# Kernel tuning notes

Measured on AMD Instinct MI355X. Metric: run time of the kernel, lower is better.

The kernel has to match this reference:

```python
import jax, jax.numpy as jnp
import numpy as np

KERNEL_SIZE = 3


def extract_local_features(feature_map, point_coords, kernel_size=KERNEL_SIZE):
    # feature_map: (B,C,H,W); point_coords: (B,N,2) normalized (y,x) in [0,1]
    B, C, H, W = feature_map.shape
    half = kernel_size // 2
    x = (point_coords[..., 1] * (W - 1)).astype(jnp.int32)  # (B,N)
    y = (point_coords[..., 0] * (H - 1)).astype(jnp.int32)
    x_min = jnp.clip(x - half, 0, None)
    x_max = jnp.clip(x + half + 1, None, W)
    y_min = jnp.clip(y - half, 0, None)
    y_max = jnpp_clip = jnp.clip(y + half + 1, None, H)
    y_max = jnp.clip(y + half + 1, None, H)
    # gather a fixed (k,k) window with clamped offsets, mask out-of-window entries
    offs = jnp.arange(kernel_size)  # (k,)
    yy = y_min[..., None] + offs  # (B,N,k) candidate rows
    xx = x_min[..., None] + offs  # (B,N,k)
    y_valid = yy < y_max[..., None]
    x_valid = xx < x_max[..., None]
    yy_c = jnp.clip(yy, 0, H - 1)
    xx_c = jnp.clip(xx, 0, W - 1)
    # flat spatial indices (B,N,k,k)
    flat_idx = yy_c[..., :, None] * W + xx_c[..., None, :]
    valid = (y_valid[..., :, None] & x_valid[..., None, :]).astype(feature_map.dtype)
    fm_flat = feature_map.reshape(B, C, H * W)  # (B,C,HW)

    def per_batch(fm, idx, val):
        # fm: (C,HW); idx,val: (N,k,k)
        g = fm[:, idx.reshape(-1)].reshape(fm.shape[0], *idx.shape)  # (C,N,k,k)
        s = jnp.einsum('cnij,nij->cn', g, val)
        cnt = val.sum(axis=(-1, -2))  # (N,)
        return s / cnt[None, :]

    return jax.vmap(per_batch)(fm_flat, flat_idx, valid)  # (B,C,N)


def point_sample(inp, point_coords):
    # bilinear grid_sample, align_corners=False, coords in [0,1] as (x,y) order
    # per the code: grid = 2*coords - 1; grid_sample uses (x,y) convention
    B, C, H, W = inp.shape
    gx = point_coords[..., 0]  # (B,N) in [0,1]
    gy = point_coords[..., 1]
    # align_corners=False mapping: pix = ((g*2-1)+1)/2 * size - 0.5 = g*size - 0.5
    fx = gx * W - 0.5
    fy = gy * H - 0.5
    x0 = jnp.floor(fx).astype(jnp.int32)
    y0 = jnp.floor(fy).astype(jnp.int32)
    wx = fx - x0
    wy = fy - y0

    def gather(yc, xc):
        inb = ((yc >= 0) & (yc < H) & (xc >= 0) & (xc < W)).astype(inp.dtype)  # (B,N)
        ycc = jnp.clip(yc, 0, H - 1)
        xcc = jnp.clip(xc, 0, W - 1)
        flat = ycc * W + xcc  # (B,N)
        fm = inp.reshape(B, C, H * W)
        g = jax.vmap(lambda f, i: f[:, i])(fm, flat)  # (B,C,N)
        return g * inb[:, None, :]

    v00 = gather(y0, x0)
    v01 = gather(y0, x0 + 1)
    v10 = gather(y0 + 1, x0)
    v11 = gather(y0 + 1, x0 + 1)
    wx_ = wx[:, None, :]
    wy_ = wy[:, None, :]
    out = (v00 * (1 - wx_) * (1 - wy_) + v01 * wx_ * (1 - wy_)
           + v10 * (1 - wx_) * wy_ + v11 * wx_ * wy_)  # (B,C,N)
    return out.transpose(0, 2, 1)  # (B,N,C)


def calculate_uncertainty(mask_logits):
    return -jnp.abs(mask_logits).squeeze(1)  # (B,H,W)


def edge_topk_sampling(edge_masks, uncertainty_map, topk):
    # edge_masks: (B,H,W) {0,1}; uncertainty_map: (B,H,W)
    B, H, W = edge_masks.shape
    NEG = jnp.asarray(-1e30, uncertainty_map.dtype)
    masked_u = jnp.where(edge_masks.reshape(B, -1) == 1,
                         uncertainty_map.reshape(B, -1), NEG)
    vals, idx = jax.lax.top_k(masked_u, topk)  # (B,topk)
    yi = (idx // W).astype(jnp.float32)
    xi = (idx % W).astype(jnp.float32)
    coords = jnp.stack([yi / (H - 1), xi / (W - 1)], axis=-1)  # (B,topk,2) (y,x)
    return idx, coords


def setup_inputs() -> dict:
    key = jax.random.key(0)
    k1, k2, k3, k4 = jax.random.split(key, 4)
    B, C, H, W = 8, 256, 256, 256
    N = 4096
    feature_map = jax.random.normal(k1, (B, C, H, W), dtype=jnp.float32)
    pred_mask = jax.random.normal(k2, (B, 1, H, W), dtype=jnp.float32)
    edge_masks = jax.random.randint(k3, (B, H, W), 0, 2).astype(jnp.int32)
    point_coords = jax.random.uniform(k4, (B, N, 2), dtype=jnp.float32)
    return {"feature_map": feature_map, "pred_mask": pred_mask,
            "edge_masks": edge_masks, "point_coords": point_coords,
            "topk": 4096}


def reference(feature_map, pred_mask, edge_masks, point_coords, topk):
    uncertainty_map = calculate_uncertainty(pred_mask)  # (B,H,W)
    idx, important_coords = edge_topk_sampling(edge_masks, uncertainty_map, topk)
    local_feats = extract_local_features(feature_map, important_coords)  # (B,C,topk)
    sampled = point_sample(feature_map, point_coords)  # (B,N,C)
    return local_feats, sampled, important_coords, idx
```

## Files before the change

kernel.cpp:

```cpp
#include <hip/hip_runtime.h>

#define CC 256
#define HH 256
#define WW 256
#define HWV 65536
#define NN 4096
#define SROWS 18
#define SSTRIDE 256

using u64 = unsigned long long;
using u32 = unsigned int;

__device__ __forceinline__ u32 lbound(const u32* __restrict__ a, u32 n, u32 key) {
    u32 lo = 0, hi = n;
    while (lo < hi) { u32 mid = (lo + hi) >> 1; if (a[mid] < key) lo = mid + 1; else hi = mid; }
    return lo;
}

__global__ void build_keys_k(const float* __restrict__ pm, const int* __restrict__ em,
                             u64* __restrict__ keys) {
    int i = blockIdx.x * blockDim.x + threadIdx.x;
    float f = (em[i] == 1) ? -fabsf(pm[i]) : -1e30f;
    u32 u = __float_as_uint(f);
    u32 k = (u & 0x80000000u) ? ~u : (u | 0x80000000u);
    u32 pix = (u32)i & 0xFFFFu;
    keys[i] = ((u64)k << 16) | (u64)(0xFFFFu - pix);
}

template<int DIRECT>
__global__ __launch_bounds__(1024) void topk_sortpc_k(const float* __restrict__ pm,
                                                      const int* __restrict__ em,
                                                      u64* __restrict__ keys,
                                                      const float* __restrict__ pc,
                                                      u32* __restrict__ stash,
                                                      u32* __restrict__ pixSorted,
                                                      u32* __restrict__ pcSorted,
                                                      float* __restrict__ outCoord,
                                                      float* __restrict__ outIdx) {
    __shared__ u64 sel[NN];
    __shared__ u64 bm[1024];
    __shared__ u32 wp[1024];
    __shared__ u32 s_digit, s_rem, s_cnt;
    const int t = threadIdx.x;
    if (blockIdx.x < 8) {
        const int b = blockIdx.x;
        u64* kb = keys + (size_t)b * HWV;
        const float* pmb = pm + (size_t)b * HWV;
        const int*   emb = em + (size_t)b * HWV;
        u32* hist = (u32*)sel;
        u64 prefix = 0ULL;
        u32 remaining = NN;
        #pragma unroll
        for (int q = 0; q < 4; ++q) hist[t + q * 1024] = 0u;
        __syncthreads();
        for (int i = t; i < HWV; i += 1024) {
            float f = (emb[i] == 1) ? -fabsf(pmb[i]) : -1e30f;
            u32 u = __float_as_uint(f);
            u32 k = (u & 0x80000000u) ? ~u : (u | 0x80000000u);
            u64 K = ((u64)k << 16) | (u64)(0xFFFFu - (u32)i);
            kb[i] = K;
            atomicAdd(&hist[(u32)(K >> 36)], 1u);
        }
        __syncthreads();
        for (int r = 0; r < 4; ++r) {
            int shift = 36 - 12 * r;
            if (r > 0) {
                #pragma unroll
                for (int q = 0; q < 4; ++q) hist[t + q * 1024] = 0u;
                __syncthreads();
                for (int i = t; i < HWV; i += 1024) {
                    u64 K = kb[i];
                    if ((K >> (shift + 12)) == prefix)
                        atomicAdd(&hist[(u32)((K >> shift) & 0xFFFULL)], 1u);
                }
                __syncthreads();
            }
            for (int off = 1; off < 4096; off <<= 1) {
                u32 v[4];
                #pragma unroll
                for (int q = 0; q < 4; ++q) {
                    int i = t + q * 1024;
                    v[q] = hist[i];
                    if (i + off < 4096) v[q] += hist[i + off];
                }
                __syncthreads();
                #pragma unroll
                for (int q = 0; q < 4; ++q) hist[t + q * 1024] = v[q];
                __syncthreads();
            }
            #pragma unroll
            for (int q = 0; q < 4; ++q) {
                int d = t + q * 1024;
                u32 ge = hist[d];
                u32 gt = (d < 4095) ? hist[d + 1] : 0u;
                if (ge >= remaining && gt < remaining) { s_digit = (u32)d; s_rem = remaining - gt; }
            }
            __syncthreads();
            prefix = (prefix << 12) | (u64)s_digit;
            remaining = s_rem;
            __syncthreads();
        }
        if (t == 0) s_cnt = 0u;
        __syncthreads();
        for (int i = t; i < HWV; i += 1024) {
            u64 K = kb[i];
            if (K >= prefix) { u32 p = atomicAdd(&s_cnt, 1u); sel[p] = K; }
        }
        __syncthreads();
        for (int k = 2; k <= NN; k <<= 1) {
            for (int j = k >> 1; j > 0; j >>= 1) {
                for (int i = t; i < NN; i += 1024) {
                    int l = i ^ j;
                    if (l > i) {
                        u64 a = sel[i], c = sel[l];
                        bool asc = ((i & k) == 0);
                        if ((a < c) == asc) { sel[i] = c; sel[l] = a; }
                    }
                }
                __syncthreads();
            }
        }
        bm[t] = 0ULL;
        __syncthreads();
        #pragma unroll
        for (int q = 0; q < 4; ++q) {
            int r = t + q * 1024;
            u32 pix = 0xFFFFu - (u32)(sel[r] & 0xFFFFULL);
            if (DIRECT) {
                u32 yi = pix >> 8, xi = pix & 255u;
                outCoord[((size_t)b * NN + r) * 2 + 0] = (float)yi / 255.0f;
                outCoord[((size_t)b * NN + r) * 2 + 1] = (float)xi / 255.0f;
                outIdx[b * NN + r] = (float)pix;
            } else {
                stash[b * NN + r] = pix;
            }
            atomicOr(&bm[pix >> 6], 1ULL << (pix & 63));
        }
        __syncthreads();
        wp[t] = (u32)__popcll(bm[t]);
        __syncthreads();
        for (int off = 1; off < 1024; off <<= 1) {
            u32 v = wp[t];
            if (t >= off) v += wp[t - off];
            __syncthreads();
            wp[t] = v;
            __syncthreads();
        }
        #pragma unroll
        for (int q = 0; q < 4; ++q) {
            int r = t + q * 1024;
            u32 pix = 0xFFFFu - (u32)(sel[r] & 0xFFFFULL);
            int w = (int)(pix >> 6);
            u32 pos = wp[w] - (u32)__popcll(bm[w])
                    + (u32)__popcll(bm[w] & ((1ULL << (pix & 63)) - 1ULL));
            pixSorted[b * NN + pos] = (pix << 12) | (u32)r;
        }
    } else {
        const int b = blockIdx.x - 8;
        u32* cellArr = (u32*)sel;
        u32* hist256 = wp;
        u32* cnt     = (u32*)bm;
        if (t < 256) { hist256[t] = 0u; cnt[t] = 0u; }
        __syncthreads();
        for (int n = t; n < NN; n += 1024) {
            float gx = pc[((size_t)b * NN + n) * 2 + 0];
            float gy = pc[((size_t)b * NN + n) * 2 + 1];
            float fx = gx * 256.0f - 0.5f;
            float fy = gy * 256.0f - 0.5f;
            int x0 = (int)floorf(fx), y0 = (int)floorf(fy);
            int xc = min(max(x0, 0), 255), yc = min(max(y0, 0), 255);
            cellArr[n] = ((u32)(yc * 256 + xc) << 12) | (u32)n;
            atomicAdd(&hist256[yc], 1u);
        }
        __syncthreads();
        for (int off = 1; off < 256; off <<= 1) {
            u32 v = 0;
            if (t < 256) { v = hist256[t]; if (t >= off) v += hist256[t - off]; }
            __syncthreads();
            if (t < 256) hist256[t] = v;
            __syncthreads();
        }
        for (int n = t; n < NN; n += 1024) {
            u32 pk = cellArr[n];
            u32 yc = pk >> 20;
            u32 base = (yc > 0) ? hist256[yc - 1] : 0u;
            u32 pos = base + atomicAdd(&cnt[yc], 1u);
            pcSorted[b * NN + pos] = pk;
        }
    }
}

#define STAGE_DMA(plane, smbuf) \
    { _Pragma("unroll") \
      for (int u = 0; u < 5; ++u) { \
        int idx = t + u * 256; \
        if (idx < SROWS * 64) { \
            int row = idx >> 6; \
            int gr = min(max(rStart + row, 0), HH - 1); \
            const float* gsrc = (plane) + gr * WW + ((idx & 63) << 2); \
            float* ldst = (smbuf) + row * SSTRIDE; \
            __builtin_amdgcn_global_load_lds( \
                (const __attribute__((address_space(1))) void*)gsrc, \
                (__attribute__((address_space(3))) void*)ldst, 16, 0, 0); \
        } } }

__global__ __launch_bounds__(256) void plane_gather_k(const float* __restrict__ fm,
                                                      const float* __restrict__ pc,
                                                      const u32* __restrict__ pixSorted,
                                                      const u32* __restrict__ pcSorted,
                                                      float* __restrict__ outLc,
                                                      float* __restrict__ outSc) {
    __shared__ float smA[SROWS * SSTRIDE];
    __shared__ float smB[SROWS * SSTRIDE];
    const int band = blockIdx.x, c0 = blockIdx.y * 32, b = blockIdx.z;
    const int t = threadIdx.x;
    const int rStart = band * 16 - 1;
    const u32 keyLo = (u32)band << 24, keyHi = (u32)(band + 1) << 24;
    const u32* aL = pixSorted + b * NN;
    const u32* aS = pcSorted + b * NN;
    u32 loL = lbound(aL, NN, keyLo), cL = lbound(aL, NN, keyHi) - loL;
    u32 loS = lbound(aS, NN, keyLo), cS = lbound(aS, NN, keyHi) - loS;
    const float* planes = fm + ((size_t)b * CC + c0) * HWV;
    const float* pcb = pc + (size_t)b * NN * 2;

    int  Lo0 = 0, Lc2 = 0, Lr2 = 0;   float Lwc = 0, Lwr = 0, Lic = 0;
    int  Mo0 = 0, Mc2 = 0, Mr2 = 0;   float Mwc = 0, Mwr = 0, Mic = 0;
    int  So0 = 0, Sr1 = 0;            float Sv0 = 0, Sv1 = 0, Sw0 = 0, Sw1 = 0;
    int  To0 = 0, Tr1 = 0;            float Tv0 = 0, Tv1 = 0, Tw0 = 0, Tw1 = 0;
    {
        u32 jl = (u32)t;
        if (jl < cL) {
            u32 pix = aL[loL + jl] >> 12;
            int yi = (int)(pix >> 8), xi = (int)(pix & 255u);
            float cy = (float)yi / 255.0f, cx = (float)xi / 255.0f;
            int x = (int)(cx * 255.0f), y = (int)(cy * 255.0f);
            int x_min = max(x - 1, 0), wid = min(x + 2, WW) - x_min;
            int y_min = max(y - 1, 0), hgt = min(y + 2, HH) - y_min;
            Lo0 = (y_min - rStart) * SSTRIDE + x_min;
            Lc2 = (wid == 3) ? 2 : 0;  Lwc = (wid == 3) ? 1.0f : 0.0f;
            Lr2 = ((hgt == 3) ? 2 : 0) * SSTRIDE;  Lwr = (hgt == 3) ? 1.0f : 0.0f;
            Lic = 1.0f / (float)(wid * hgt);
        }
        jl = 256u + (u32)t;
        if (jl < cL) {
            u32 pix = aL[loL + jl] >> 12;
            int yi = (int)(pix >> 8), xi = (int)(pix & 255u);
            float cy = (float)yi / 255.0f, cx = (float)xi / 255.0f;
            int x = (int)(cx * 255.0f), y = (int)(cy * 255.0f);
            int x_min = max(x - 1, 0), wid = min(x + 2, WW) - x_min;
            int y_min = max(y - 1, 0), hgt = min(y + 2, HH) - y_min;
            Mo0 = (y_min - rStart) * SSTRIDE + x_min;
            Mc2 = (wid == 3) ? 2 : 0;  Mwc = (wid == 3) ? 1.0f : 0.0f;
            Mr2 = ((hgt == 3) ? 2 : 0) * SSTRIDE;  Mwr = (hgt == 3) ? 1.0f : 0.0f;
            Mic = 1.0f / (float)(wid * hgt);
        }
        u32 js = (u32)t;
        if (js < cS) {
            u32 sn = aS[loS + js] & 0xFFFu;
            float gx = pcb[2 * sn + 0], gy = pcb[2 * sn + 1];
            float fx = gx * 256.0f - 0.5f, fy = gy * 256.0f - 0.5f;
            float fx0 = floorf(fx), fy0 = floorf(fy);
            int x0 = (int)fx0, y0 = (int)fy0;
            float wx = fx - fx0, wy = fy - fy0;
            int xb = min(max(x0, 0), WW - 2);
            if (x0 < 0)            { Sv0 = wx;        Sv1 = 0.0f; }
            else if (x0 >= WW - 1) { Sv0 = 0.0f;      Sv1 = 1.0f - wx; }
            else                   { Sv0 = 1.0f - wx; Sv1 = wx; }
            Sw0 = (y0 >= 0)     ? (1.0f - wy) : 0.0f;
            Sw1 = (y0 + 1 < HH) ? wy          : 0.0f;
            int yc0 = min(max(y0, 0), HH - 1), yc1 = min(max(y0 + 1, 0), HH - 1);
            So0 = (yc0 - rStart) * SSTRIDE + xb;
            Sr1 = (yc1 - yc0) * SSTRIDE;
        }
        js = 256u + (u32)t;
        if (js < cS) {
            u32 sn = aS[loS + js] & 0xFFFu;
            float gx = pcb[2 * sn + 0], gy = pcb[2 * sn + 1];
            float fx = gx * 256.0f - 0.5f, fy = gy * 256.0f - 0.5f;
            float fx0 = floorf(fx), fy0 = floorf(fy);
            int x0 = (int)fx0, y0 = (int)fy0;
            float wx = fx - fx0, wy = fy - fy0;
            int xb = min(max(x0, 0), WW - 2);
            if (x0 < 0)            { Tv0 = wx;        Tv1 = 0.0f; }
            else if (x0 >= WW - 1) { Tv0 = 0.0f;      Tv1 = 1.0f - wx; }
            else                   { Tv0 = 1.0f - wx; Tv1 = wx; }
            Tw0 = (y0 >= 0)     ? (1.0f - wy) : 0.0f;
            Tw1 = (y0 + 1 < HH) ? wy          : 0.0f;
            int yc0 = min(max(y0, 0), HH - 1), yc1 = min(max(y0 + 1, 0), HH - 1);
            To0 = (yc0 - rStart) * SSTRIDE + xb;
            Tr1 = (yc1 - yc0) * SSTRIDE;
        }
    }

    STAGE_DMA(planes, smA)
    __syncthreads();

    #pragma unroll 1
    for (int j = 0; j < 32; ++j) {
        const float* sm = (j & 1) ? smB : smA;
        if (j + 1 < 32) {
            const float* np = planes + (size_t)(j + 1) * HWV;
            float* nb = ((j + 1) & 1) ? smB : smA;
            STAGE_DMA(np, nb)
        }
        float* oL = outLc + ((size_t)(b * CC + c0 + j)) * NN + loL;
        float* oS = outSc + ((size_t)(b * CC + c0 + j)) * NN + loS;
        if ((u32)t < cL) {
            float r0 = sm[Lo0] + sm[Lo0 + 1] + Lwc * sm[Lo0 + Lc2];
            float r1 = sm[Lo0 + SSTRIDE] + sm[Lo0 + SSTRIDE + 1] + Lwc * sm[Lo0 + SSTRIDE + Lc2];
            int o2 = Lo0 + Lr2;
            float r2 = sm[o2] + sm[o2 + 1] + Lwc * sm[o2 + Lc2];
            oL[t] = (r0 + r1 + Lwr * r2) * Lic;
        }
        if (256u + (u32)t < cL) {
            float r0 = sm[Mo0] + sm[Mo0 + 1] + Mwc * sm[Mo0 + Mc2];
            float r1 = sm[Mo0 + SSTRIDE] + sm[Mo0 + SSTRIDE + 1] + Mwc * sm[Mo0 + SSTRIDE + Mc2];
            int o2 = Mo0 + Mr2;
            float r2 = sm[o2] + sm[o2 + 1] + Mwc * sm[o2 + Mc2];
            oL[256 + t] = (r0 + r1 + Mwr * r2) * Mic;
        }
        if ((u32)t < cS) {
            oS[t] = Sw0 * (sm[So0] * Sv0 + sm[So0 + 1] * Sv1)
                  + Sw1 * (sm[So0 + Sr1] * Sv0 + sm[So0 + Sr1 + 1] * Sv1);
        }
        if (256u + (u32)t < cS) {
            oS[256 + t] = Tw0 * (sm[To0] * Tv0 + sm[To0 + 1] * Tv1)
                        + Tw1 * (sm[To0 + Tr1] * Tv0 + sm[To0 + Tr1 + 1] * Tv1);
        }
        __syncthreads();
    }

    for (u32 jl = 512 + (u32)t; jl < cL; jl += 256) {
        u32 pix = aL[loL + jl] >> 12;
        int yi = (int)(pix >> 8), xi = (int)(pix & 255u);
        float cy = (float)yi / 255.0f, cx = (float)xi / 255.0f;
        int x = (int)(cx * 255.0f), y = (int)(cy * 255.0f);
        int x_min = max(x - 1, 0), x_max = min(x + 2, WW);
        int y_min = max(y - 1, 0), y_max = min(y + 2, HH);
        float ic = 1.0f / (float)((x_max - x_min) * (y_max - y_min));
        for (int j = 0; j < 32; ++j) {
            const float* p = planes + (size_t)j * HWV;
            float s = 0.0f;
            for (int yy = y_min; yy < y_max; ++yy)
                for (int xx = x_min; xx < x_max; ++xx) s += p[yy * WW + xx];
            outLc[((size_t)(b * CC + c0 + j)) * NN + loL + jl] = s * ic;
        }
    }
    for (u32 js = 512 + (u32)t; js < cS; js += 256) {
        u32 sn = aS[loS + js] & 0xFFFu;
        float gx = pcb[2 * sn + 0], gy = pcb[2 * sn + 1];
        float fx = gx * 256.0f - 0.5f, fy = gy * 256.0f - 0.5f;
        float fx0 = floorf(fx), fy0 = floorf(fy);
        int x0 = (int)fx0, y0 = (int)fy0;
        float wx = fx - fx0, wy = fy - fy0;
        int xb = min(max(x0, 0), WW - 2);
        float v0, v1, r0, r1;
        if (x0 < 0)            { v0 = wx;        v1 = 0.0f; }
        else if (x0 >= WW - 1) { v0 = 0.0f;      v1 = 1.0f - wx; }
        else                   { v0 = 1.0f - wx; v1 = wx; }
        r0 = (y0 >= 0)     ? (1.0f - wy) : 0.0f;
        r1 = (y0 + 1 < HH) ? wy          : 0.0f;
        int yc0 = min(max(y0, 0), HH - 1), yc1 = min(max(y0 + 1, 0), HH - 1);
        int o0 = yc0 * WW + xb, o1 = yc1 * WW + xb;
        for (int j = 0; j < 32; ++j) {
            const float* p = planes + (size_t)j * HWV;
            outSc[((size_t)(b * CC + c0 + j)) * NN + loS + js] =
                r0 * (p[o0] * v0 + p[o0 + 1] * v1) + r1 * (p[o1] * v0 + p[o1 + 1] * v1);
        }
    }
}

__global__ __launch_bounds__(256) void unpermL_k(const float* __restrict__ outLc,
                                                 const u32* __restrict__ pixSorted,
                                                 float* __restrict__ outL) {
    __shared__ float row[NN];
    const int c = blockIdx.x, b = blockIdx.y;
    const int t = threadIdx.x;
    const float* in = outLc + ((size_t)(b * CC + c)) * NN;
    for (int j = t; j < NN; j += 256)
        row[pixSorted[b * NN + j] & 0xFFFu] = in[j];
    __syncthreads();
    float* o = outL + ((size_t)(b * CC + c)) * NN;
    for (int i = t; i < NN; i += 256) o[i] = row[i];
}

__global__ __launch_bounds__(256) void unpermS_k(const float* __restrict__ outSc,
                                                 const u32* __restrict__ pcSorted,
                                                 float* __restrict__ outS) {
    __shared__ float tile[32][257];
    __shared__ u32 ns[256];
    const int j0 = blockIdx.x * 256, c0 = blockIdx.y * 32, b = blockIdx.z;
    const int t = threadIdx.x;
    ns[t] = pcSorted[b * NN + j0 + t] & 0xFFFu;
    for (int i = 0; i < 32; ++i)
        tile[i][t] = outSc[((size_t)(b * CC + c0 + i)) * NN + j0 + t];
    __syncthreads();
    for (int idx = t; idx < 8192; idx += 256) {
        int p = idx >> 5, k = idx & 31;
        outS[((size_t)b * NN + ns[p]) * CC + c0 + k] = tile[k][p];
    }
}

template<int DIRECT>
__global__ __launch_bounds__(1024) void topk_sortpc_old_k(const u64* __restrict__ keys,
                                                          const float* __restrict__ pc,
                                                          u32* __restrict__ stash,
                                                          u32* __restrict__ pixSorted,
                                                          u32* __restrict__ pcSorted,
                                                          float* __restrict__ outCoord,
                                                          float* __restrict__ outIdx) {
    __shared__ u64 sel[NN];
    __shared__ u64 bm[1024];
    __shared__ u32 wp[1024];
    __shared__ u32 s_digit, s_rem, s_cnt;
    const int t = threadIdx.x;
    if (blockIdx.x < 8) {
        const int b = blockIdx.x;
        const u64* kb = keys + (size_t)b * HWV;
        u32* hist = (u32*)sel;
        u64 prefix = 0ULL;
        u32 remaining = NN;
        for (int r = 0; r < 4; ++r) {
            int shift = 36 - 12 * r;
            #pragma unroll
            for (int q = 0; q < 4; ++q) hist[t + q * 1024] = 0u;
            __syncthreads();
            for (int i = t; i < HWV; i += 1024) {
                u64 K = kb[i];
                if ((K >> (shift + 12)) == prefix)
                    atomicAdd(&hist[(u32)((K >> shift) & 0xFFFULL)], 1u);
            }
            __syncthreads();
            for (int off = 1; off < 4096; off <<= 1) {
                u32 v[4];
                #pragma unroll
                for (int q = 0; q < 4; ++q) {
                    int i = t + q * 1024;
                    v[q] = hist[i];
                    if (i + off < 4096) v[q] += hist[i + off];
                }
                __syncthreads();
                #pragma unroll
                for (int q = 0; q < 4; ++q) hist[t + q * 1024] = v[q];
                __syncthreads();
            }
            #pragma unroll
            for (int q = 0; q < 4; ++q) {
                int d = t + q * 1024;
                u32 ge = hist[d];
                u32 gt = (d < 4095) ? hist[d + 1] : 0u;
                if (ge >= remaining && gt < remaining) { s_digit = (u32)d; s_rem = remaining - gt; }
            }
            __syncthreads();
            prefix = (prefix << 12) | (u64)s_digit;
            remaining = s_rem;
            __syncthreads();
        }
        if (t == 0) s_cnt = 0u;
        __syncthreads();
        for (int i = t; i < HWV; i += 1024) {
            u64 K = kb[i];
            if (K >= prefix) { u32 p = atomicAdd(&s_cnt, 1u); sel[p] = K; }
        }
        __syncthreads();
        for (int k = 2; k <= NN; k <<= 1) {
            for (int j = k >> 1; j > 0; j >>= 1) {
                for (int i = t; i < NN; i += 1024) {
                    int l = i ^ j;
                    if (l > i) {
                        u64 a = sel[i], c = sel[l];
                        bool asc = ((i & k) == 0);
                        if ((a < c) == asc) { sel[i] = c; sel[l] = a; }
                    }
                }
                __syncthreads();
            }
        }
        bm[t] = 0ULL;
        __syncthreads();
        #pragma unroll
        for (int q = 0; q < 4; ++q) {
            int r = t + q * 1024;
            u32 pix = 0xFFFFu - (u32)(sel[r] & 0xFFFFULL);
            if (DIRECT) {
                u32 yi = pix >> 8, xi = pix & 255u;
                outCoord[((size_t)b * NN + r) * 2 + 0] = (float)yi / 255.0f;
                outCoord[((size_t)b * NN + r) * 2 + 1] = (float)xi / 255.0f;
                outIdx[b * NN + r] = (float)pix;
            } else {
                stash[b * NN + r] = pix;
            }
            atomicOr(&bm[pix >> 6], 1ULL << (pix & 63));
        }
        __syncthreads();
        wp[t] = (u32)__popcll(bm[t]);
        __syncthreads();
        for (int off = 1; off < 1024; off <<= 1) {
            u32 v = wp[t];
            if (t >= off) v += wp[t - off];
            __syncthreads();
            wp[t] = v;
            __syncthreads();
        }
        #pragma unroll
        for (int q = 0; q < 4; ++q) {
            int r = t + q * 1024;
            u32 pix = 0xFFFFu - (u32)(sel[r] & 0xFFFFULL);
            int w = (int)(pix >> 6);
            u32 pos = wp[w] - (u32)__popcll(bm[w])
                    + (u32)__popcll(bm[w] & ((1ULL << (pix & 63)) - 1ULL));
            pixSorted[b * NN + pos] = (pix << 12) | (u32)r;
        }
    } else {
        const int b = blockIdx.x - 8;
        u32* cellArr = (u32*)sel;
        u32* hist256 = wp;
        u32* cnt     = (u32*)bm;
        if (t < 256) { hist256[t] = 0u; cnt[t] = 0u; }
        __syncthreads();
        for (int n = t; n < NN; n += 1024) {
            float gx = pc[((size_t)b * NN + n) * 2 + 0];
            float gy = pc[((size_t)b * NN + n) * 2 + 1];
            float fx = gx * 256.0f - 0.5f;
            float fy = gy * 256.0f - 0.5f;
            int x0 = (int)floorf(fx), y0 = (int)floorf(fy);
            int xc = min(max(x0, 0), 255), yc = min(max(y0, 0), 255);
            cellArr[n] = ((u32)(yc * 256 + xc) << 12) | (u32)n;
            atomicAdd(&hist256[yc], 1u);
        }
        __syncthreads();
        for (int off = 1; off < 256; off <<= 1) {
            u32 v = 0;
            if (t < 256) { v = hist256[t]; if (t >= off) v += hist256[t - off]; }
            __syncthreads();
            if (t < 256) hist256[t] = v;
            __syncthreads();
        }
        for (int n = t; n < NN; n += 1024) {
            u32 pk = cellArr[n];
            u32 yc = pk >> 20;
            u32 base = (yc > 0) ? hist256[yc - 1] : 0u;
            u32 pos = base + atomicAdd(&cnt[yc], 1u);
            pcSorted[b * NN + pos] = pk;
        }
    }
}

template<int MODE>
__global__ __launch_bounds__(256, 4) void gather_k(const float* __restrict__ fm,
                                                   const float* __restrict__ pc,
                                                   const u32* __restrict__ pixSorted,
                                                   const u32* __restrict__ pcSorted,
                                                   float* __restrict__ outLp,
                                                   float* __restrict__ outS) {
    __shared__ float tile[256][33];
    __shared__ u32 pidx[256];
    const int b = blockIdx.z, j0 = blockIdx.x * 256, t = threadIdx.x;
    bool doL; int c0;
    if (MODE == 1) { doL = true; c0 = blockIdx.y * 32; }
    else { doL = false; c0 = blockIdx.y * 32; }
    const float* planes = fm + ((size_t)b * CC + c0) * HWV;
    if (doL) {
        u32 packed = pixSorted[b * NN + j0 + t];
        u32 pix = packed >> 12;
        pidx[t] = packed & 0xFFFu;
        int yi = (int)(pix >> 8), xi = (int)(pix & 255u);
        float cy = (float)yi / 255.0f, cx = (float)xi / 255.0f;
        int x = (int)(cx * 255.0f), y = (int)(cy * 255.0f);
        int x_min = max(x - 1, 0), x_max = min(x + 2, WW);
        int y_min = max(y - 1, 0), y_max = min(y + 2, HH);
        int base = min(x_min & ~3, WW - 8);
        float w8[8];
        #pragma unroll
        for (int i = 0; i < 8; ++i)
            w8[i] = (base + i >= x_min && base + i < x_max) ? 1.0f : 0.0f;
        float wr2 = (y_min + 2 < y_max) ? 1.0f : 0.0f;
        int o0 = y_min * WW + base, o1 = o0 + WW;
        int o2 = min(y_min + 2, HH - 1) * WW + base;
        float invc = 1.0f / (float)((x_max - x_min) * (y_max - y_min));
        #pragma unroll 2
        for (int j = 0; j < 32; ++j) {
            const float* p = planes + (size_t)j * HWV;
            float4 a0 = *(const float4*)(p + o0), b0 = *(const float4*)(p + o0 + 4);
            float4 a1 = *(const float4*)(p + o1), b1 = *(const float4*)(p + o1 + 4);
            float4 a2 = *(const float4*)(p + o2), b2 = *(const float4*)(p + o2 + 4);
            float s0 = a0.x * w8[0] + a0.y * w8[1] + a0.z * w8[2] + a0.w * w8[3]
                     + b0.x * w8[4] + b0.y * w8[5] + b0.z * w8[6] + b0.w * w8[7];
            float s1 = a1.x * w8[0] + a1.y * w8[1] + a1.z * w8[2] + a1.w * w8[3]
                     + b1.x * w8[4] + b1.y * w8[5] + b1.z * w8[6] + b1.w * w8[7];
            float s2 = a2.x * w8[0] + a2.y * w8[1] + a2.z * w8[2] + a2.w * w8[3]
                     + b2.x * w8[4] + b2.y * w8[5] + b2.z * w8[6] + b2.w * w8[7];
            tile[t][j] = (s0 + s1 + wr2 * s2) * invc;
        }
        __syncthreads();
        for (int idx = t; idx < 8192; idx += 256) {
            int p = idx >> 5, k = idx & 31;
            outLp[((size_t)b * NN + pidx[p]) * CC + c0 + k] = tile[p][k];
        }
    } else {
        int n = (int)(pcSorted[b * NN + j0 + t] & 0xFFFu);
        pidx[t] = (u32)n;
        float gx = pc[((size_t)b * NN + n) * 2 + 0];
        float gy = pc[((size_t)b * NN + n) * 2 + 1];
        float fx = gx * 256.0f - 0.5f, fy = gy * 256.0f - 0.5f;
        float fx0 = floorf(fx), fy0 = floorf(fy);
        int x0 = (int)fx0, y0 = (int)fy0;
        float wx = fx - fx0, wy = fy - fy0;
        int xb = min(max(x0, 0), WW - 2);
        float wv0, wv1;
        if (x0 < 0)            { wv0 = wx;        wv1 = 0.0f; }
        else if (x0 >= WW - 1) { wv0 = 0.0f;      wv1 = 1.0f - wx; }
        else                   { wv0 = 1.0f - wx; wv1 = wx; }
        float wr0 = (y0 >= 0)     ? (1.0f - wy) : 0.0f;
        float wr1 = (y0 + 1 < HH) ? wy          : 0.0f;
        int yc0 = min(max(y0, 0), HH - 1), yc1 = min(max(y0 + 1, 0), HH - 1);
        int o0 = yc0 * WW + xb, o1 = yc1 * WW + xb;
        #pragma unroll 4
        for (int j = 0; j < 32; ++j) {
            const float* p = planes + (size_t)j * HWV;
            tile[t][j] = wr0 * (p[o0] * wv0 + p[o0 + 1] * wv1)
                       + wr1 * (p[o1] * wv0 + p[o1 + 1] * wv1);
        }
        __syncthreads();
        for (int idx = t; idx < 8192; idx += 256) {
            int p = idx >> 5, k = idx & 31;
            outS[((size_t)b * NN + pidx[p]) * CC + c0 + k] = tile[p][k];
        }
    }
}

__global__ __launch_bounds__(256) void transpose_k(const float* __restrict__ outLp,
                                                   float* __restrict__ outL) {
    __shared__ float tile[256][33];
    const int b = blockIdx.z, c0 = blockIdx.y * 32, r0 = blockIdx.x * 256;
    const int t = threadIdx.x;
    for (int idx = t; idx < 8192; idx += 256) {
        int p = idx >> 5, k = idx & 31;
        tile[p][k] = outLp[((size_t)b * NN + r0 + p) * CC + c0 + k];
    }
    __syncthreads();
    for (int idx = t; idx < 8192; idx += 256) {
        int cl = idx >> 8, col = idx & 255;
        outL[((size_t)b * CC + c0 + cl) * NN + r0 + col] = tile[col][cl];
    }
}

__global__ void emit_k(const u32* __restrict__ stash, float* __restrict__ outCoord,
                       float* __restrict__ outIdx) {
    int i = blockIdx.x * blockDim.x + threadIdx.x;
    u32 p = stash[i];
    u32 yi = p >> 8, xi = p & 255u;
    outCoord[(size_t)i * 2 + 0] = (float)yi / 255.0f;
    outCoord[(size_t)i * 2 + 1] = (float)xi / 255.0f;
    outIdx[i] = (float)p;
}

extern "C" void kernel_launch(void* const* d_in, const int* in_sizes, int n_in,
                              void* d_out, int out_size, void* d_ws, size_t ws_size,
                              hipStream_t stream) {
    const float* fm = (const float*)d_in[0];
    const float* pm = (const float*)d_in[1];
    const int*   em = (const int*)d_in[2];
    const float* pc = (const float*)d_in[3];
    (void)in_sizes; (void)n_in; (void)out_size;

    float* out      = (float*)d_out;
    float* outL     = out;
    float* outS     = out + (size_t)8388608;
    float* outCoord = out + (size_t)16777216;
    float* outIdx   = out + (size_t)16842752;

    const size_t need_ws = (size_t)80 * 1024 * 1024;
    bool ws_ok = ws_size >= need_ws;

    if (ws_ok) {
        char* w = (char*)d_ws;
        u64* keys      = (u64*)w;
        u32* pixSorted = (u32*)(w + (size_t)4300 * 1024);
        u32* pcSorted  = (u32*)(w + (size_t)4600 * 1024);
        float* outLc   = (float*)(w + (size_t)5  * 1024 * 1024);
        float* outSc   = (float*)(w + (size_t)40 * 1024 * 1024);

        hipLaunchKernelGGL((topk_sortpc_k<1>), dim3(16), dim3(1024), 0, stream,
                           pm, em, keys, pc, (u32*)nullptr, pixSorted, pcSorted,
                           outCoord, outIdx);
        hipLaunchKernelGGL(plane_gather_k, dim3(16, 8, 8), dim3(256), 0, stream,
                           fm, pc, pixSorted, pcSorted, outLc, outSc);
        hipLaunchKernelGGL(unpermL_k, dim3(256, 8), dim3(256), 0, stream,
                           outLc, pixSorted, outL);
        hipLaunchKernelGGL(unpermS_k, dim3(16, 8, 8), dim3(256), 0, stream,
                           outSc, pcSorted, outS);
    } else {
        u64* keys      = (u64*)outS;
        u32* stash     = (u32*)outIdx;
        u32* pixSorted = (u32*)outCoord;
        u32* pcSorted  = pixSorted + 32768;
        float* outLp   = outS;

        hipLaunchKernelGGL(build_keys_k, dim3(2048), dim3(256), 0, stream, pm, em, keys);
        hipLaunchKernelGGL((topk_sortpc_old_k<0>), dim3(16), dim3(1024), 0, stream,
                           keys, pc, stash, pixSorted, pcSorted, outCoord, outIdx);
        hipLaunchKernelGGL((gather_k<1>), dim3(16, 8, 8), dim3(256), 0, stream,
                           fm, pc, pixSorted, pcSorted, outLp, outS);
        hipLaunchKernelGGL(transpose_k, dim3(16, 8, 8), dim3(256), 0, stream, outLp, outL);
        hipLaunchKernelGGL((gather_k<2>), dim3(16, 8, 8), dim3(256), 0, stream,
                           fm, pc, pixSorted, pcSorted, outS, outS);
        hipLaunchKernelGGL(emit_k, dim3(128), dim3(256), 0, stream, stash, outCoord, outIdx);
    }
}
```

Before: 368.8 us.

## Parallelize key build and first histogram; register-staged plane loads with padded LDS

Moves key construction and the first-pass radix histogram out of the 8-block top-k kernel into a 2048-block kernel that builds shared histograms and merges them into global memory with atomics, so that the top-k kernel starts from a precomputed histogram. The plane gather kernel replaces double-buffered global-to-LDS DMA with register-staged float4 loads into a single padded LDS buffer (stride 260), written after compute behind an extra barrier. The 3x3 window reads become vectorized float2 reads with per-column weight masks. The change adds two kernel launches and one more barrier per channel, and it gives up the direct async LDS loads.

```diff
diff --git a/kernel.cpp b/kernel.cpp
--- a/kernel.cpp
+++ b/kernel.cpp
@@ -6,7 +6,7 @@
 #define HWV 65536
 #define NN 4096
 #define SROWS 18
-#define SSTRIDE 256
+#define SSTRIDE 260
 
 using u64 = unsigned long long;
 using u32 = unsigned int;
@@ -17,22 +17,39 @@
     return lo;
 }
 
-__global__ void build_keys_k(const float* __restrict__ pm, const int* __restrict__ em,
-                             u64* __restrict__ keys) {
-    int i = blockIdx.x * blockDim.x + threadIdx.x;
+__global__ void zero_hist_k(u32* __restrict__ ghist) {
+    ghist[blockIdx.x * 1024 + threadIdx.x] = 0u;
+}
+
+__global__ __launch_bounds__(256) void build_keys_hist_k(const float* __restrict__ pm,
+                                                         const int* __restrict__ em,
+                                                         u64* __restrict__ keys,
+                                                         u32* __restrict__ ghist) {
+    __shared__ u32 h[4096];
+    const int t = threadIdx.x;
+    #pragma unroll
+    for (int q = 0; q < 16; ++q) h[t + q * 256] = 0u;
+    __syncthreads();
+    int i = blockIdx.x * 256 + t;
+    int b = i >> 16;
     float f = (em[i] == 1) ? -fabsf(pm[i]) : -1e30f;
     u32 u = __float_as_uint(f);
     u32 k = (u & 0x80000000u) ? ~u : (u | 0x80000000u);
-    u32 pix = (u32)i & 0xFFFFu;
-    keys[i] = ((u64)k << 16) | (u64)(0xFFFFu - pix);
-}
-
-template<int DIRECT>
-__global__ __launch_bounds__(1024) void topk_sortpc_k(const float* __restrict__ pm,
-                                                      const int* __restrict__ em,
-                                                      u64* __restrict__ keys,
+    u64 K = ((u64)k << 16) | (u64)(0xFFFFu - ((u32)i & 0xFFFFu));
+    keys[i] = K;
+    atomicAdd(&h[(u32)(K >> 36)], 1u);
+    __syncthreads();
+    u32* gh = ghist + b * 4096;
+    #pragma unroll
+    for (int q = 0; q < 16; ++q) {
+        u32 v = h[t + q * 256];
+        if (v) atomicAdd(&gh[t + q * 256], v);
+    }
+}
+
+__global__ __launch_bounds__(1024) void topk_sortpc_k(const u64* __restrict__ keys,
+                                                      const u32* __restrict__ ghist,
                                                       const float* __restrict__ pc,
-                                                      u32* __restrict__ stash,
                                                       u32* __restrict__ pixSorted,
                                                       u32* __restrict__ pcSorted,
                                                       float* __restrict__ outCoord,
@@ -44,27 +61,17 @@
     const int t = threadIdx.x;
     if (blockIdx.x < 8) {
         const int b = blockIdx.x;
-        u64* kb = keys + (size_t)b * HWV;
-        const float* pmb = pm + (size_t)b * HWV;
-        const int*   emb = em + (size_t)b * HWV;
+        const u64* kb = keys + (size_t)b * HWV;
         u32* hist = (u32*)sel;
         u64 prefix = 0ULL;
         u32 remaining = NN;
-        #pragma unroll
-        for (int q = 0; q < 4; ++q) hist[t + q * 1024] = 0u;
-        __syncthreads();
-        for (int i = t; i < HWV; i += 1024) {
-            float f = (emb[i] == 1) ? -fabsf(pmb[i]) : -1e30f;
-            u32 u = __float_as_uint(f);
-            u32 k = (u & 0x80000000u) ? ~u : (u | 0x80000000u);
-            u64 K = ((u64)k << 16) | (u64)(0xFFFFu - (u32)i);
-            kb[i] = K;
-            atomicAdd(&hist[(u32)(K >> 36)], 1u);
-        }
-        __syncthreads();
         for (int r = 0; r < 4; ++r) {
             int shift = 36 - 12 * r;
-            if (r > 0) {
+            if (r == 0) {
+                #pragma unroll
+                for (int q = 0; q < 4; ++q) hist[t + q * 1024] = ghist[b * 4096 + t + q * 1024];
+                __syncthreads();
+            } else {
                 #pragma unroll
                 for (int q = 0; q < 4; ++q) hist[t + q * 1024] = 0u;
                 __syncthreads();
@@ -126,14 +133,10 @@
         for (int q = 0; q < 4; ++q) {
             int r = t + q * 1024;
             u32 pix = 0xFFFFu - (u32)(sel[r] & 0xFFFFULL);
-            if (DIRECT) {
-                u32 yi = pix >> 8, xi = pix & 255u;
-                outCoord[((size_t)b * NN + r) * 2 + 0] = (float)yi / 255.0f;
-                outCoord[((size_t)b * NN + r) * 2 + 1] = (float)xi / 255.0f;
-                outIdx[b * NN + r] = (float)pix;
-            } else {
-                stash[b * NN + r] = pix;
-            }
+            u32 yi = pix >> 8, xi = pix & 255u;
+            outCoord[((size_t)b * NN + r) * 2 + 0] = (float)yi / 255.0f;
+            outCoord[((size_t)b * NN + r) * 2 + 1] = (float)xi / 255.0f;
+            outIdx[b * NN + r] = (float)pix;
             atomicOr(&bm[pix >> 6], 1ULL << (pix & 63));
         }
         __syncthreads();
@@ -190,19 +193,26 @@
     }
 }
 
-#define STAGE_DMA(plane, smbuf) \
-    { _Pragma("unroll") \
-      for (int u = 0; u < 5; ++u) { \
-        int idx = t + u * 256; \
-        if (idx < SROWS * 64) { \
-            int row = idx >> 6; \
-            int gr = min(max(rStart + row, 0), HH - 1); \
-            const float* gsrc = (plane) + gr * WW + ((idx & 63) << 2); \
-            float* ldst = (smbuf) + row * SSTRIDE; \
-            __builtin_amdgcn_global_load_lds( \
-                (const __attribute__((address_space(1))) void*)gsrc, \
-                (__attribute__((address_space(3))) void*)ldst, 16, 0, 0); \
-        } } }
+#define STAGE_LOAD(plane) \
+    { int idx, r, c4, gr; \
+      idx = t;        r = idx >> 6; c4 = idx & 63; gr = min(max(rStart + r, 0), HH - 1); \
+      g0 = *(const float4*)((plane) + gr * WW + c4 * 4); \
+      idx = t + 256;  r = idx >> 6; c4 = idx & 63; gr = min(max(rStart + r, 0), HH - 1); \
+      g1 = *(const float4*)((plane) + gr * WW + c4 * 4); \
+      idx = t + 512;  r = idx >> 6; c4 = idx & 63; gr = min(max(rStart + r, 0), HH - 1); \
+      g2 = *(const float4*)((plane) + gr * WW + c4 * 4); \
+      idx = t + 768;  r = idx >> 6; c4 = idx & 63; gr = min(max(rStart + r, 0), HH - 1); \
+      g3 = *(const float4*)((plane) + gr * WW + c4 * 4); \
+      if (t < 128) { idx = t + 1024; r = idx >> 6; c4 = idx & 63; gr = min(max(rStart + r, 0), HH - 1); \
+      g4 = *(const float4*)((plane) + gr * WW + c4 * 4); } }
+
+#define STAGE_WRITE() \
+    { int idx, r, c4; \
+      idx = t;        r = idx >> 6; c4 = idx & 63; *(float4*)(sm + r * SSTRIDE + c4 * 4) = g0; \
+      idx = t + 256;  r = idx >> 6; c4 = idx & 63; *(float4*)(sm + r * SSTRIDE + c4 * 4) = g1; \
+      idx = t + 512;  r = idx >> 6; c4 = idx & 63; *(float4*)(sm + r * SSTRIDE + c4 * 4) = g2; \
+      idx = t + 768;  r = idx >> 6; c4 = idx & 63; *(float4*)(sm + r * SSTRIDE + c4 * 4) = g3; \
+      if (t < 128) { idx = t + 1024; r = idx >> 6; c4 = idx & 63; *(float4*)(sm + r * SSTRIDE + c4 * 4) = g4; } }
 
 __global__ __launch_bounds__(256) void plane_gather_k(const float* __restrict__ fm,
                                                       const float* __restrict__ pc,
@@ -210,8 +220,7 @@
                                                       const u32* __restrict__ pcSorted,
                                                       float* __restrict__ outLc,
                                                       float* __restrict__ outSc) {
-    __shared__ float smA[SROWS * SSTRIDE];
-    __shared__ float smB[SROWS * SSTRIDE];
+    __shared__ float sm[SROWS * SSTRIDE];
     const int band = blockIdx.x, c0 = blockIdx.y * 32, b = blockIdx.z;
     const int t = threadIdx.x;
     const int rStart = band * 16 - 1;
@@ -223,10 +232,10 @@
     const float* planes = fm + ((size_t)b * CC + c0) * HWV;
     const float* pcb = pc + (size_t)b * NN * 2;
 
-    int  Lo0 = 0, Lc2 = 0, Lr2 = 0;   float Lwc = 0, Lwr = 0, Lic = 0;
-    int  Mo0 = 0, Mc2 = 0, Mr2 = 0;   float Mwc = 0, Mwr = 0, Mic = 0;
-    int  So0 = 0, Sr1 = 0;            float Sv0 = 0, Sv1 = 0, Sw0 = 0, Sw1 = 0;
-    int  To0 = 0, Tr1 = 0;            float Tv0 = 0, Tv1 = 0, Tw0 = 0, Tw1 = 0;
+    int  Lo0 = 0, Lr2 = 0;  float Lw0 = 0, Lw1 = 0, Lw2 = 0, Lw3 = 0, Lwr = 0, Lic = 0;
+    int  Mo0 = 0, Mr2 = 0;  float Mw0 = 0, Mw1 = 0, Mw2 = 0, Mw3 = 0, Mwr = 0, Mic = 0;
+    int  So0 = 0, Sr1 = 0;  float Sv0 = 0, Sv1 = 0, Sw0 = 0, Sw1 = 0;
+    int  To0 = 0, Tr1 = 0;  float Tv0 = 0, Tv1 = 0, Tw0 = 0, Tw1 = 0;
     {
         u32 jl = (u32)t;
         if (jl < cL) {
@@ -234,12 +243,16 @@
             int yi = (int)(pix >> 8), xi = (int)(pix & 255u);
             float cy = (float)yi / 255.0f, cx = (float)xi / 255.0f;
             int x = (int)(cx * 255.0f), y = (int)(cy * 255.0f);
-            int x_min = max(x - 1, 0), wid = min(x + 2, WW) - x_min;
+            int x_min = max(x - 1, 0), x_max = min(x + 2, WW);
             int y_min = max(y - 1, 0), hgt = min(y + 2, HH) - y_min;
-            Lo0 = (y_min - rStart) * SSTRIDE + x_min;
-            Lc2 = (wid == 3) ? 2 : 0;  Lwc = (wid == 3) ? 1.0f : 0.0f;
+            int base2 = min(x_min & ~1, WW - 4);
+            Lw0 = (base2 + 0 >= x_min && base2 + 0 < x_max) ? 1.0f : 0.0f;
+            Lw1 = (base2 + 1 >= x_min && base2 + 1 < x_max) ? 1.0f : 0.0f;
+            Lw2 = (base2 + 2 >= x_min && base2 + 2 < x_max) ? 1.0f : 0.0f;
+            Lw3 = (base2 + 3 >= x_min && base2 + 3 < x_max) ? 1.0f : 0.0f;
+            Lo0 = (y_min - rStart) * SSTRIDE + base2;
             Lr2 = ((hgt == 3) ? 2 : 0) * SSTRIDE;  Lwr = (hgt == 3) ? 1.0f : 0.0f;
-            Lic = 1.0f / (float)(wid * hgt);
+            Lic = 1.0f / (float)((x_max - x_min) * hgt);
         }
         jl = 256u + (u32)t;
         if (jl < cL) {
@@ -247,12 +260,16 @@
             int yi = (int)(pix >> 8), xi = (int)(pix & 255u);
             float cy = (float)yi / 255.0f, cx = (float)xi / 255.0f;
             int x = (int)(cx * 255.0f), y = (int)(cy * 255.0f);
-            int x_min = max(x - 1, 0), wid = min(x + 2, WW) - x_min;
+            int x_min = max(x - 1, 0), x_max = min(x + 2, WW);
             int y_min = max(y - 1, 0), hgt = min(y + 2, HH) - y_min;
-            Mo0 = (y_min - rStart) * SSTRIDE + x_min;
-            Mc2 = (wid == 3) ? 2 : 0;  Mwc = (wid == 3) ? 1.0f : 0.0f;
+            int base2 = min(x_min & ~1, WW - 4);
+            Mw0 = (base2 + 0 >= x_min && base2 + 0 < x_max) ? 1.0f : 0.0f;
+            Mw1 = (base2 + 1 >= x_min && base2 + 1 < x_max) ? 1.0f : 0.0f;
+            Mw2 = (base2 + 2 >= x_min && base2 + 2 < x_max) ? 1.0f : 0.0f;
+            Mw3 = (base2 + 3 >= x_min && base2 + 3 < x_max) ? 1.0f : 0.0f;
+            Mo0 = (y_min - rStart) * SSTRIDE + base2;
             Mr2 = ((hgt == 3) ? 2 : 0) * SSTRIDE;  Mwr = (hgt == 3) ? 1.0f : 0.0f;
-            Mic = 1.0f / (float)(wid * hgt);
+            Mic = 1.0f / (float)((x_max - x_min) * hgt);
         }
         u32 js = (u32)t;
         if (js < cS) {
@@ -292,31 +309,38 @@
         }
     }
 
-    STAGE_DMA(planes, smA)
+    float4 g0, g1, g2, g3, g4;
+    STAGE_LOAD(planes)
+    STAGE_WRITE()
     __syncthreads();
 
     #pragma unroll 1
     for (int j = 0; j < 32; ++j) {
-        const float* sm = (j & 1) ? smB : smA;
-        if (j + 1 < 32) {
-            const float* np = planes + (size_t)(j + 1) * HWV;
-            float* nb = ((j + 1) & 1) ? smB : smA;
-            STAGE_DMA(np, nb)
-        }
+        if (j + 1 < 32) { const float* np = planes + (size_t)(j + 1) * HWV; STAGE_LOAD(np) }
         float* oL = outLc + ((size_t)(b * CC + c0 + j)) * NN + loL;
         float* oS = outSc + ((size_t)(b * CC + c0 + j)) * NN + loS;
         if ((u32)t < cL) {
-            float r0 = sm[Lo0] + sm[Lo0 + 1] + Lwc * sm[Lo0 + Lc2];
-            float r1 = sm[Lo0 + SSTRIDE] + sm[Lo0 + SSTRIDE + 1] + Lwc * sm[Lo0 + SSTRIDE + Lc2];
-            int o2 = Lo0 + Lr2;
-            float r2 = sm[o2] + sm[o2 + 1] + Lwc * sm[o2 + Lc2];
+            float2 a0 = *(const float2*)(sm + Lo0);
+            float2 b0 = *(const float2*)(sm + Lo0 + 2);
+            float2 a1 = *(const float2*)(sm + Lo0 + SSTRIDE);
+            float2 b1 = *(const float2*)(sm + Lo0 + SSTRIDE + 2);
+            float2 a2 = *(const float2*)(sm + Lo0 + Lr2);
+            float2 b2 = *(const float2*)(sm + Lo0 + Lr2 + 2);
+            float r0 = a0.x * Lw0 + a0.y * Lw1 + b0.x * Lw2 + b0.y * Lw3;
+            float r1 = a1.x * Lw0 + a1.y * Lw1 + b1.x * Lw2 + b1.y * Lw3;
+            float r2 = a2.x * Lw0 + a2.y * Lw1 + b2.x * Lw2 + b2.y * Lw3;
             oL[t] = (r0 + r1 + Lwr * r2) * Lic;
         }
         if (256u + (u32)t < cL) {
-            float r0 = sm[Mo0] + sm[Mo0 + 1] + Mwc * sm[Mo0 + Mc2];
-            float r1 = sm[Mo0 + SSTRIDE] + sm[Mo0 + SSTRIDE + 1] + Mwc * sm[Mo0 + SSTRIDE + Mc2];
-            int o2 = Mo0 + Mr2;
-            float r2 = sm[o2] + sm[o2 + 1] + Mwc * sm[o2 + Mc2];
+            float2 a0 = *(const float2*)(sm + Mo0);
+            float2 b0 = *(const float2*)(sm + Mo0 + 2);
+            float2 a1 = *(const float2*)(sm + Mo0 + SSTRIDE);
+            float2 b1 = *(const float2*)(sm + Mo0 + SSTRIDE + 2);
+            float2 a2 = *(const float2*)(sm + Mo0 + Mr2);
+            float2 b2 = *(const float2*)(sm + Mo0 + Mr2 + 2);
+            float r0 = a0.x * Mw0 + a0.y * Mw1 + b0.x * Mw2 + b0.y * Mw3;
+            float r1 = a1.x * Mw0 + a1.y * Mw1 + b1.x * Mw2 + b1.y * Mw3;
+            float r2 = a2.x * Mw0 + a2.y * Mw1 + b2.x * Mw2 + b2.y * Mw3;
             oL[256 + t] = (r0 + r1 + Mwr * r2) * Mic;
         }
         if ((u32)t < cS) {
@@ -327,6 +351,8 @@
             oS[256 + t] = Tw0 * (sm[To0] * Tv0 + sm[To0 + 1] * Tv1)
                         + Tw1 * (sm[To0 + Tr1] * Tv0 + sm[To0 + Tr1 + 1] * Tv1);
         }
+        __syncthreads();
+        if (j + 1 < 32) { STAGE_WRITE() }
         __syncthreads();
     }
 
@@ -401,14 +427,21 @@
     }
 }
 
-template<int DIRECT>
+__global__ void build_keys_k(const float* __restrict__ pm, const int* __restrict__ em,
+                             u64* __restrict__ keys) {
+    int i = blockIdx.x * blockDim.x + threadIdx.x;
+    float f = (em[i] == 1) ? -fabsf(pm[i]) : -1e30f;
+    u32 u = __float_as_uint(f);
+    u32 k = (u & 0x80000000u) ? ~u : (u | 0x80000000u);
+    u32 pix = (u32)i & 0xFFFFu;
+    keys[i] = ((u64)k << 16) | (u64)(0xFFFFu - pix);
+}
+
 __global__ __launch_bounds__(1024) void topk_sortpc_old_k(const u64* __restrict__ keys,
                                                           const float* __restrict__ pc,
                                                           u32* __restrict__ stash,
                                                           u32* __restrict__ pixSorted,
-                                                          u32* __restrict__ pcSorted,
-                                                          float* __restrict__ outCoord,
-                                                          float* __restrict__ outIdx) {
+                                                          u32* __restrict__ pcSorted) {
     __shared__ u64 sel[NN];
     __shared__ u64 bm[1024];
     __shared__ u32 wp[1024];
@@ -482,14 +515,7 @@
         for (int q = 0; q < 4; ++q) {
             int r = t + q * 1024;
             u32 pix = 0xFFFFu - (u32)(sel[r] & 0xFFFFULL);
-            if (DIRECT) {
-                u32 yi = pix >> 8, xi = pix & 255u;
-                outCoord[((size_t)b * NN + r) * 2 + 0] = (float)yi / 255.0f;
-                outCoord[((size_t)b * NN + r) * 2 + 1] = (float)xi / 255.0f;
-                outIdx[b * NN + r] = (float)pix;
-            } else {
-                stash[b * NN + r] = pix;
-            }
+            stash[b * NN + r] = pix;
             atomicOr(&bm[pix >> 6], 1ULL << (pix & 63));
         }
         __syncthreads();
@@ -556,9 +582,7 @@
     __shared__ float tile[256][33];
     __shared__ u32 pidx[256];
     const int b = blockIdx.z, j0 = blockIdx.x * 256, t = threadIdx.x;
-    bool doL; int c0;
-    if (MODE == 1) { doL = true; c0 = blockIdx.y * 32; }
-    else { doL = false; c0 = blockIdx.y * 32; }
+    bool doL = (MODE == 1); int c0 = blockIdx.y * 32;
     const float* planes = fm + ((size_t)b * CC + c0) * HWV;
     if (doL) {
         u32 packed = pixSorted[b * NN + j0 + t];
@@ -676,14 +700,17 @@
     if (ws_ok) {
         char* w = (char*)d_ws;
         u64* keys      = (u64*)w;
+        u32* ghist     = (u32*)(w + (size_t)4096 * 1024);
         u32* pixSorted = (u32*)(w + (size_t)4300 * 1024);
         u32* pcSorted  = (u32*)(w + (size_t)4600 * 1024);
         float* outLc   = (float*)(w + (size_t)5  * 1024 * 1024);
         float* outSc   = (float*)(w + (size_t)40 * 1024 * 1024);
 
-        hipLaunchKernelGGL((topk_sortpc_k<1>), dim3(16), dim3(1024), 0, stream,
-                           pm, em, keys, pc, (u32*)nullptr, pixSorted, pcSorted,
-                           outCoord, outIdx);
+        hipLaunchKernelGGL(zero_hist_k, dim3(32), dim3(1024), 0, stream, ghist);
+        hipLaunchKernelGGL(build_keys_hist_k, dim3(2048), dim3(256), 0, stream,
+                           pm, em, keys, ghist);
+        hipLaunchKernelGGL(topk_sortpc_k, dim3(16), dim3(1024), 0, stream,
+                           keys, ghist, pc, pixSorted, pcSorted, outCoord, outIdx);
         hipLaunchKernelGGL(plane_gather_k, dim3(16, 8, 8), dim3(256), 0, stream,
                            fm, pc, pixSorted, pcSorted, outLc, outSc);
         hipLaunchKernelGGL(unpermL_k, dim3(256, 8), dim3(256), 0, stream,
@@ -698,8 +725,8 @@
         float* outLp   = outS;
 
         hipLaunchKernelGGL(build_keys_k, dim3(2048), dim3(256), 0, stream, pm, em, keys);
-        hipLaunchKernelGGL((topk_sortpc_old_k<0>), dim3(16), dim3(1024), 0, stream,
-                           keys, pc, stash, pixSorted, pcSorted, outCoord, outIdx);
+        hipLaunchKernelGGL(topk_sortpc_old_k, dim3(16), dim3(1024), 0, stream,
+                           keys, pc, stash, pixSorted, pcSorted);
         hipLaunchKernelGGL((gather_k<1>), dim3(16, 8, 8), dim3(256), 0, stream,
                            fm, pc, pixSorted, pcSorted, outLp, outS);
         hipLaunchKernelGGL(transpose_k, dim3(16, 8, 8), dim3(256), 0, stream, outLp, outL);
```

After: 311.2 us, median of 2. 15.6% less time.
